# Performance work log

Hardware: AMD Instinct MI355X
Metric: run time of the kernel (lower is better)

The kernel has to match this reference:

```python
import jax, jax.numpy as jnp
import numpy as np

# layer dims: 30->24->19->14->10->6->2->1
_DIMS = [30, 24, 19, 14, 10, 6, 2, 1]


def setup_inputs() -> dict:
    key = jax.random.key(0)
    ks = jax.random.split(key, 1 + 2 * (len(_DIMS) - 1))
    inp = {"x": jax.random.normal(ks[0], (1048576, 30), dtype=jnp.float32)}
    for i in range(len(_DIMS) - 1):
        fan_in, fan_out = _DIMS[i], _DIMS[i + 1]
        bound = 1.0 / np.sqrt(fan_in)
        inp[f"W{i+1}"] = jax.random.uniform(ks[1 + 2 * i], (fan_out, fan_in), dtype=jnp.float32, minval=-bound, maxval=bound)
        inp[f"b{i+1}"] = jax.random.uniform(ks[2 + 2 * i], (fan_out,), dtype=jnp.float32, minval=-bound, maxval=bound)
    return inp


def reference(x, W1, b1, W2, b2, W3, b3, W4, b4, W5, b5, W6, b6, W7, b7):
    # 6 Linear+ReLU layers, then final Linear (no activation)
    for W, b in [(W1, b1), (W2, b2), (W3, b3), (W4, b4), (W5, b5), (W6, b6)]:
        x = jax.nn.relu(x @ W.T + b)
    return x @ W7.T + b7
```

## Files before the change

kernel.cpp:

```cpp
#include <hip/hip_runtime.h>


#define NTHREADS 256

typedef __fp16       h2     __attribute__((ext_vector_type(2)));
typedef __fp16       half8  __attribute__((ext_vector_type(8)));
typedef float        f32x16 __attribute__((ext_vector_type(16)));
typedef unsigned int uint4v __attribute__((ext_vector_type(4)));

__device__ __forceinline__ h2 cpk(float a, float b) {
    return __builtin_bit_cast(h2, __builtin_amdgcn_cvt_pkrtz(a, b));
}
__device__ __forceinline__ h2 relu2(h2 v) {
    h2 z = {(__fp16)0.f, (__fp16)0.f};
#if __has_builtin(__builtin_elementwise_max)
    return __builtin_elementwise_max(v, z);
#else
    v.x = v.x > (__fp16)0.f ? v.x : (__fp16)0.f;
    v.y = v.y > (__fp16)0.f ? v.y : (__fp16)0.f;
    return v;
#endif
}
__device__ __forceinline__ unsigned ucast(h2 v) { return __builtin_bit_cast(unsigned, v); }

__device__ __forceinline__ f32x16 mfma_(half8 A, half8 B, f32x16 C) {
    return __builtin_amdgcn_mfma_f32_32x32x16_f16(A, B, C, 0, 0, 0);
}

template <int FIN, int FOUT, int KPAD>
__device__ __forceinline__ void stageW(const float* __restrict__ W, const float* __restrict__ B,
                                       __fp16* __restrict__ sbase, int t) {
    for (int idx = t; idx < 32 * KPAD; idx += NTHREADS) {
        int m = idx / KPAD;
        int k = idx & (KPAD - 1);
        float v = 0.f;
        if (m < FOUT) {
            if (k < FIN) v = W[m * FIN + k];
            else if (k == FIN) v = B[m];
        }
        int byte = idx * 2;
        byte ^= (m & 7) << 4;
        *(__fp16*)((char*)sbase + byte) = (__fp16)v;
    }
}

__device__ __forceinline__ half8 ldA(const __fp16* base, int KPAD, int ks, int lane) {
    int m = lane & 31;
    int byte = (m * KPAD + ks * 16 + ((lane >> 5) & 1) * 8) * 2;
    byte ^= (m & 7) << 4;
    return __builtin_bit_cast(half8, *(const uint4v*)((const char*)base + byte));
}

template <int R, int POS>
__device__ __forceinline__ half8 bfrag(const f32x16& d, int lane) {
    unsigned u0 = ucast(relu2(cpk(d[R + 0], d[R + 1])));
    unsigned u1 = ucast(relu2(cpk(d[R + 2], d[R + 3])));
    unsigned u2 = ucast(relu2(cpk(d[R + 4], d[R + 5])));
    unsigned u3 = ucast(relu2(cpk(d[R + 6], d[R + 7])));
    bool lo = (lane & 32) == 0;
    unsigned s0 = __shfl_xor(u0, 32), s1 = __shfl_xor(u1, 32);
    unsigned s2 = __shfl_xor(u2, 32), s3 = __shfl_xor(u3, 32);
    unsigned w0 = lo ? u0 : s2;
    unsigned w1 = lo ? u1 : s3;
    unsigned w2 = lo ? s0 : u2;
    unsigned w3 = lo ? s1 : u3;
    if constexpr (POS >= 0) {
        constexpr bool hiT = POS >= 8;
        constexpr int  p   = POS & 7;
        constexpr unsigned bits = (p & 1) ? 0x3C000000u : 0x00003C00u;
        bool sel = (((lane & 32) != 0) == hiT);
        unsigned ob = sel ? bits : 0u;
        if constexpr ((p >> 1) == 0) w0 |= ob;
        else if constexpr ((p >> 1) == 1) w1 |= ob;
        else if constexpr ((p >> 1) == 2) w2 |= ob;
        else w3 |= ob;
    }
    uint4v u = {w0, w1, w2, w3};
    return __builtin_bit_cast(half8, u);
}

__device__ __forceinline__ half8 packx(unsigned a, unsigned b, unsigned c, unsigned d) {
    uint4v u = {a, b, c, d};
    return __builtin_bit_cast(half8, u);
}

#define SLABS 4

__global__ __launch_bounds__(NTHREADS, 3) void mlp_mfma2(
    const float* __restrict__ x,
    const float* __restrict__ W1, const float* __restrict__ B1,
    const float* __restrict__ W2, const float* __restrict__ B2,
    const float* __restrict__ W3, const float* __restrict__ B3,
    const float* __restrict__ W4, const float* __restrict__ B4,
    const float* __restrict__ W5, const float* __restrict__ B5,
    const float* __restrict__ W6, const float* __restrict__ B6,
    const float* __restrict__ W7, const float* __restrict__ B7,
    float* __restrict__ out, int nrows)
{
    __shared__ __align__(16) __fp16 shw[5120];
    __shared__ __align__(16) float  sx[2][3840];

    const int t    = threadIdx.x;
    const int lane = t & 63;
    const int wid  = t >> 6;
    const int hb   = (lane >> 5) & 1;

    stageW<30, 24, 32>(W1, B1, shw + 0,    t);
    stageW<24, 19, 32>(W2, B2, shw + 1024, t);
    stageW<19, 14, 32>(W3, B3, shw + 2048, t);
    stageW<14, 10, 16>(W4, B4, shw + 3072, t);
    stageW<10, 6,  16>(W5, B5, shw + 3584, t);
    stageW<6,  2,  16>(W6, B6, shw + 4096, t);
    stageW<2,  1,  16>(W7, B7, shw + 4608, t);

    {
        const float4* gx = (const float4*)(x + (size_t)blockIdx.x * (SLABS * 3840));
        float4* s0 = (float4*)sx[0];
        for (int i = t; i < 960; i += NTHREADS) s0[i] = gx[i];
    }
    __syncthreads();

    const half8 A10 = ldA(shw + 0,    32, 0, lane), A11 = ldA(shw + 0,    32, 1, lane);
    const half8 A20 = ldA(shw + 1024, 32, 0, lane), A21 = ldA(shw + 1024, 32, 1, lane);
    const half8 A30 = ldA(shw + 2048, 32, 0, lane), A31 = ldA(shw + 2048, 32, 1, lane);
    const half8 A4  = ldA(shw + 3072, 16, 0, lane);
    const half8 A5  = ldA(shw + 3584, 16, 0, lane);
    const half8 A6  = ldA(shw + 4096, 16, 0, lane);
    const half8 A7  = ldA(shw + 4608, 16, 0, lane);

    const f32x16 z = {0.f,0.f,0.f,0.f, 0.f,0.f,0.f,0.f, 0.f,0.f,0.f,0.f, 0.f,0.f,0.f,0.f};

    for (int s = 0; s < SLABS; ++s) {
        float4 pf0, pf1, pf2, pf3;
        const bool hp3 = t < (960 - 3 * NTHREADS);
        if (s < SLABS - 1) {
            const float4* gx = (const float4*)(x + ((size_t)blockIdx.x * SLABS + s + 1) * 3840);
            pf0 = gx[t];
            pf1 = gx[t + NTHREADS];
            pf2 = gx[t + 2 * NTHREADS];
            if (hp3) pf3 = gx[t + 3 * NTHREADS];
        }

        const float* xs = sx[s & 1];
        const float* xr = xs + (wid * 32 + (lane & 31)) * 30;
        float f0a[8], f1a[8];
        {
            const float2* p0 = (const float2*)(xr + hb * 8);
            float2 a = p0[0], b = p0[1], c = p0[2], d = p0[3];
            f0a[0] = a.x; f0a[1] = a.y; f0a[2] = b.x; f0a[3] = b.y;
            f0a[4] = c.x; f0a[5] = c.y; f0a[6] = d.x; f0a[7] = d.y;
            const float2* p1 = (const float2*)(xr + 16 + hb * 8);
            float2 e = p1[0], g = p1[1], h = p1[2], i = p1[3];
            f1a[0] = e.x; f1a[1] = e.y; f1a[2] = g.x; f1a[3] = g.y;
            f1a[4] = h.x; f1a[5] = h.y; f1a[6] = i.x; f1a[7] = i.y;
        }
        half8 Bx0 = packx(ucast(cpk(f0a[0], f0a[1])), ucast(cpk(f0a[2], f0a[3])),
                          ucast(cpk(f0a[4], f0a[5])), ucast(cpk(f0a[6], f0a[7])));
        unsigned x13 = hb ? 0x00003C00u : ucast(cpk(f1a[6], f1a[7]));
        half8 Bx1 = packx(ucast(cpk(f1a[0], f1a[1])), ucast(cpk(f1a[2], f1a[3])),
                          ucast(cpk(f1a[4], f1a[5])), x13);

        f32x16 a1 = mfma_(A10, Bx0, z);
        a1 = mfma_(A11, Bx1, a1);
        f32x16 a2 = mfma_(A20, bfrag<0, -1>(a1, lane), z);
        a2 = mfma_(A21, bfrag<8, 8>(a1, lane), a2);
        f32x16 a3 = mfma_(A30, bfrag<0, -1>(a2, lane), z);
        a3 = mfma_(A31, bfrag<8, 3>(a2, lane), a3);
        f32x16 a4 = mfma_(A4, bfrag<0, 14>(a3, lane), z);
        f32x16 a5 = mfma_(A5, bfrag<0, 10>(a4, lane), z);
        f32x16 a6 = mfma_(A6, bfrag<0, 6>(a5, lane), z);
        f32x16 a7 = mfma_(A7, bfrag<0, 2>(a6, lane), z);

        const int row0 = (blockIdx.x * SLABS + s) * 128 + wid * 32;
        if (lane < 32) {
            int r = row0 + lane;
            if (r < nrows) out[r] = a7[0];
        }

        if (s < SLABS - 1) {
            float4* so = (float4*)sx[(s + 1) & 1];
            so[t] = pf0;
            so[t + NTHREADS] = pf1;
            so[t + 2 * NTHREADS] = pf2;
            if (hp3) so[t + 3 * NTHREADS] = pf3;
        }
        __syncthreads();
    }
}

extern "C" void kernel_launch(void* const* d_in, const int* in_sizes, int n_in,
                              void* d_out, int out_size, void* d_ws, size_t ws_size,
                              hipStream_t stream) {
    const float* x = (const float*)d_in[0];
    int nrows = in_sizes[0] / 30;
    int blocks = (nrows + SLABS * 128 - 1) / (SLABS * 128);
    mlp_mfma2<<<blocks, NTHREADS, 0, stream>>>(
        x,
        (const float*)d_in[1],  (const float*)d_in[2],
        (const float*)d_in[3],  (const float*)d_in[4],
        (const float*)d_in[5],  (const float*)d_in[6],
        (const float*)d_in[7],  (const float*)d_in[8],
        (const float*)d_in[9],  (const float*)d_in[10],
        (const float*)d_in[11], (const float*)d_in[12],
        (const float*)d_in[13], (const float*)d_in[14],
        (float*)d_out, nrows);
}
```

Baseline: 35.11 us.

## Give each wavefront a private LDS tile buffer and drop block-wide barriers

Each of the four wavefronts now owns its own 32-row tile sequence and a private LDS staging buffer, replacing the block-shared double buffer that needed a __syncthreads per slab. Register prefetch of the next tile is issued after the current tile is read from LDS, so loads overlap the MFMA chain without block synchronisation. LDS use drops from two 3840-float buffers to four 960-float ones. Correctness of the write-then-read through LDS within a wave now relies on intra-wave ordering with no explicit wave barrier.

```diff
diff --git a/kernel.cpp b/kernel.cpp
--- a/kernel.cpp
+++ b/kernel.cpp
@@ -2,6 +2,7 @@
 
 
 #define NTHREADS 256
+#define TPW 4
 
 typedef __fp16       h2     __attribute__((ext_vector_type(2)));
 typedef __fp16       half8  __attribute__((ext_vector_type(8)));
@@ -84,9 +85,7 @@
     return __builtin_bit_cast(half8, u);
 }
 
-#define SLABS 4
-
-__global__ __launch_bounds__(NTHREADS, 3) void mlp_mfma2(
+__global__ __launch_bounds__(NTHREADS, 3) void mlp_mfma3(
     const float* __restrict__ x,
     const float* __restrict__ W1, const float* __restrict__ B1,
     const float* __restrict__ W2, const float* __restrict__ B2,
@@ -98,7 +97,7 @@
     float* __restrict__ out, int nrows)
 {
     __shared__ __align__(16) __fp16 shw[5120];
-    __shared__ __align__(16) float  sx[2][3840];
+    __shared__ __align__(16) float  sxw[4][960];
 
     const int t    = threadIdx.x;
     const int lane = t & 63;
@@ -112,12 +111,6 @@
     stageW<10, 6,  16>(W5, B5, shw + 3584, t);
     stageW<6,  2,  16>(W6, B6, shw + 4096, t);
     stageW<2,  1,  16>(W7, B7, shw + 4608, t);
-
-    {
-        const float4* gx = (const float4*)(x + (size_t)blockIdx.x * (SLABS * 3840));
-        float4* s0 = (float4*)sx[0];
-        for (int i = t; i < 960; i += NTHREADS) s0[i] = gx[i];
-    }
     __syncthreads();
 
     const half8 A10 = ldA(shw + 0,    32, 0, lane), A11 = ldA(shw + 0,    32, 1, lane);
@@ -130,19 +123,27 @@
 
     const f32x16 z = {0.f,0.f,0.f,0.f, 0.f,0.f,0.f,0.f, 0.f,0.f,0.f,0.f, 0.f,0.f,0.f,0.f};
 
-    for (int s = 0; s < SLABS; ++s) {
-        float4 pf0, pf1, pf2, pf3;
-        const bool hp3 = t < (960 - 3 * NTHREADS);
-        if (s < SLABS - 1) {
-            const float4* gx = (const float4*)(x + ((size_t)blockIdx.x * SLABS + s + 1) * 3840);
-            pf0 = gx[t];
-            pf1 = gx[t + NTHREADS];
-            pf2 = gx[t + 2 * NTHREADS];
-            if (hp3) pf3 = gx[t + 3 * NTHREADS];
-        }
-
-        const float* xs = sx[s & 1];
-        const float* xr = xs + (wid * 32 + (lane & 31)) * 30;
+    const int tile0 = (blockIdx.x * 4 + wid) * TPW;
+    float4* wb = (float4*)sxw[wid];
+
+    float4 pf0, pf1, pf2, pf3;
+    {
+        const float4* gx = (const float4*)x + (size_t)tile0 * 240;
+        pf0 = gx[lane];
+        pf1 = gx[lane + 64];
+        pf2 = gx[lane + 128];
+        if (lane < 48) pf3 = gx[lane + 192];
+    }
+
+    for (int it = 0; it < TPW; ++it) {
+        const int T = tile0 + it;
+
+        wb[lane]       = pf0;
+        wb[lane + 64]  = pf1;
+        wb[lane + 128] = pf2;
+        if (lane < 48) wb[lane + 192] = pf3;
+
+        const float* xr = sxw[wid] + (lane & 31) * 30;
         float f0a[8], f1a[8];
         {
             const float2* p0 = (const float2*)(xr + hb * 8);
@@ -160,6 +161,14 @@
         half8 Bx1 = packx(ucast(cpk(f1a[0], f1a[1])), ucast(cpk(f1a[2], f1a[3])),
                           ucast(cpk(f1a[4], f1a[5])), x13);
 
+        if (it + 1 < TPW) {
+            const float4* gx = (const float4*)x + (size_t)(T + 1) * 240;
+            pf0 = gx[lane];
+            pf1 = gx[lane + 64];
+            pf2 = gx[lane + 128];
+            if (lane < 48) pf3 = gx[lane + 192];
+        }
+
         f32x16 a1 = mfma_(A10, Bx0, z);
         a1 = mfma_(A11, Bx1, a1);
         f32x16 a2 = mfma_(A20, bfrag<0, -1>(a1, lane), z);
@@ -171,20 +180,11 @@
         f32x16 a6 = mfma_(A6, bfrag<0, 6>(a5, lane), z);
         f32x16 a7 = mfma_(A7, bfrag<0, 2>(a6, lane), z);
 
-        const int row0 = (blockIdx.x * SLABS + s) * 128 + wid * 32;
+        const int row0 = T * 32;
         if (lane < 32) {
             int r = row0 + lane;
             if (r < nrows) out[r] = a7[0];
         }
-
-        if (s < SLABS - 1) {
-            float4* so = (float4*)sx[(s + 1) & 1];
-            so[t] = pf0;
-            so[t + NTHREADS] = pf1;
-            so[t + 2 * NTHREADS] = pf2;
-            if (hp3) so[t + 3 * NTHREADS] = pf3;
-        }
-        __syncthreads();
     }
 }
 
@@ -193,8 +193,9 @@
                               hipStream_t stream) {
     const float* x = (const float*)d_in[0];
     int nrows = in_sizes[0] / 30;
-    int blocks = (nrows + SLABS * 128 - 1) / (SLABS * 128);
-    mlp_mfma2<<<blocks, NTHREADS, 0, stream>>>(
+    int rows_per_block = 4 * TPW * 32;
+    int blocks = (nrows + rows_per_block - 1) / rows_per_block;
+    mlp_mfma3<<<blocks, NTHREADS, 0, stream>>>(
         x,
         (const float*)d_in[1],  (const float*)d_in[2],
         (const float*)d_in[3],  (const float*)d_in[4],
```

Result: no change. 35.47 us (+1.0%).
